# Kernel optimization log

Measured on AMD Instinct MI355X. Metric: run time of the kernel, lower is better.

The kernel has to match this reference:

```python
import jax, jax.numpy as jnp
import numpy as np

DIM = 96; NH = 3; WS = 7; SHIFT = 3; P = 5; H = 56; W = 56
HEAD = DIM // NH; SCALE = HEAD ** -0.5
NWH = H // WS; NWW = W // WS; NW = NWH * NWW
TP = P * NW                 # total prompts = 320
N = P + WS * WS             # tokens per window incl. prompts = 54
HIDDEN = int(DIM * 4.0)


def _rel_pos_index():
    coords = np.stack(np.meshgrid(np.arange(WS), np.arange(WS), indexing='ij'))
    cf = coords.reshape(2, -1)
    rel = (cf[:, :, None] - cf[:, None, :]).transpose(1, 2, 0).astype(np.int64)
    rel[..., 0] += WS - 1
    rel[..., 1] += WS - 1
    rel[..., 0] *= 2 * WS - 1
    return rel.sum(-1)  # (49, 49)


def _attn_mask():
    img = np.zeros((H, W))
    cnt = 0
    sl = (slice(0, -WS), slice(-WS, -SHIFT), slice(-SHIFT, None))
    for hs in sl:
        for wsl in sl:
            img[hs, wsl] = cnt
            cnt += 1
    mw = img.reshape(NWH, WS, NWW, WS).transpose(0, 2, 1, 3).reshape(NW, WS * WS)
    am = mw[:, None, :] - mw[:, :, None]
    am = np.where(am != 0, -100.0, 0.0).astype(np.float32)
    # zero-pad for prompt rows/cols, matching the torch code's cat of zeros
    return np.pad(am, ((0, 0), (P, 0), (P, 0)))  # (NW, N, N)


RPI = _rel_pos_index()
MASK = jnp.asarray(_attn_mask())


def _ln(x, g, b):
    m = x.mean(-1, keepdims=True)
    v = ((x - m) ** 2).mean(-1, keepdims=True)
    return (x - m) / jnp.sqrt(v + 1e-5) * g + b


def setup_inputs() -> dict:
    key = jax.random.key(0)
    ks = jax.random.split(key, 10)
    B = 64
    s = DIM ** -0.5
    return {
        'x': jax.random.normal(ks[0], (B, H * W + TP, DIM), jnp.float32),
        'norm1_g': jnp.ones((DIM,), jnp.float32),
        'norm1_b': jnp.zeros((DIM,), jnp.float32),
        'qkv_w': jax.random.normal(ks[1], (DIM, 3 * DIM), jnp.float32) * s,
        'qkv_b': jnp.zeros((3 * DIM,), jnp.float32),
        'rpb_table': jax.random.normal(ks[2], ((2 * WS - 1) ** 2, NH), jnp.float32) * 0.02,
        'proj_w': jax.random.normal(ks[3], (DIM, DIM), jnp.float32) * s,
        'proj_b': jnp.zeros((DIM,), jnp.float32),
        'norm2_g': jnp.ones((DIM,), jnp.float32),
        'norm2_b': jnp.zeros((DIM,), jnp.float32),
        'fc1_w': jax.random.normal(ks[4], (DIM, HIDDEN), jnp.float32) * s,
        'fc1_b': jnp.zeros((HIDDEN,), jnp.float32),
        'fc2_w': jax.random.normal(ks[5], (HIDDEN, DIM), jnp.float32) * (HIDDEN ** -0.5),
        'fc2_b': jnp.zeros((DIM,), jnp.float32),
    }


def _block(x, norm1_g, norm1_b, qkv_w, qkv_b, rpb_table, proj_w, proj_b,
           norm2_g, norm2_b, fc1_w, fc1_b, fc2_w, fc2_b):
    B = x.shape[0]
    shortcut = x
    xn = _ln(x, norm1_g, norm1_b)

    prompt = xn[:, :TP, :]                       # (B, NW*P, C)
    feat = xn[:, TP:, :].reshape(B, H, W, DIM)
    feat = jnp.roll(feat, (-SHIFT, -SHIFT), (1, 2))

    # window partition -> (B*NW, WS*WS, C)
    xw = feat.reshape(B, NWH, WS, NWW, WS, DIM).transpose(0, 1, 3, 2, 4, 5)
    xw = xw.reshape(B * NW, WS * WS, DIM)
    # prepend per-window prompts
    xw = jnp.concatenate([prompt.reshape(B * NW, P, DIM), xw], axis=1)  # (B*NW, N, C)

    # attention
    qkv = (xw @ qkv_w + qkv_b).reshape(B * NW, N, 3, NH, HEAD).transpose(2, 0, 3, 1, 4)
    q, k, v = qkv[0] * SCALE, qkv[1], qkv[2]     # (B*NW, NH, N, HEAD)
    attn = jnp.einsum('bhnd,bhmd->bhnm', q, k)

    bias = rpb_table[RPI.reshape(-1)].reshape(WS * WS, WS * WS, NH).transpose(2, 0, 1)
    bias = jnp.pad(bias, ((0, 0), (P, 0), (P, 0)))  # (NH, N, N)
    attn = attn + bias[None]

    attn = attn.reshape(B, NW, NH, N, N) + MASK[None, :, None]
    attn = jax.nn.softmax(attn.reshape(B * NW, NH, N, N), axis=-1)

    out = jnp.einsum('bhnm,bhmd->bhnd', attn, v).transpose(0, 2, 1, 3).reshape(B * NW, N, DIM)
    out = out @ proj_w + proj_b

    prompt_out = out[:, :P, :].reshape(B, TP, DIM)
    fo = out[:, P:, :].reshape(B, NWH, NWW, WS, WS, DIM).transpose(0, 1, 3, 2, 4, 5)
    fo = fo.reshape(B, H, W, DIM)
    fo = jnp.roll(fo, (SHIFT, SHIFT), (1, 2))

    y = jnp.concatenate([prompt_out, fo.reshape(B, H * W, DIM)], axis=1)
    y = shortcut + y

    h = _ln(y, norm2_g, norm2_b)
    h = jax.nn.gelu(h @ fc1_w + fc1_b, approximate=False)
    y = y + (h @ fc2_w + fc2_b)
    return y


def reference(x, norm1_g, norm1_b, qkv_w, qkv_b, rpb_table, proj_w, proj_b,
              norm2_g, norm2_b, fc1_w, fc1_b, fc2_w, fc2_b):
    return _block(x, norm1_g, norm1_b, qkv_w, qkv_b, rpb_table, proj_w, proj_b,
                  norm2_g, norm2_b, fc1_w, fc1_b, fc2_w, fc2_b)
```

## Files before the change

kernel.cpp:

```cpp
#include <hip/hip_runtime.h>
#include <cmath>

typedef __bf16 bf16x8 __attribute__((ext_vector_type(8)));
typedef __bf16 bf16x4 __attribute__((ext_vector_type(4)));
typedef float  f32x4  __attribute__((ext_vector_type(4)));

#define MFMA16(a,b,c) __builtin_amdgcn_mfma_f32_16x16x32_bf16((a),(b),(c),0,0,0)

#define SCALE_Q 0.17677669529663687f


#define KST 104
#define VP  68


__global__ __launch_bounds__(256) void prep(const float* __restrict__ qkv_w,
                                            const float* __restrict__ proj_w,
                                            const float* __restrict__ fc1_w,
                                            const float* __restrict__ fc2_w,
                                            const float* __restrict__ rpb,
                                            __bf16* __restrict__ ws,
                                            float* __restrict__ tbl)
{
    int i = blockIdx.x * 256 + threadIdx.x;
    {
        int j = i;
        if (j < 27648) {
            int c = j / 96, k = j % 96;
            float v = qkv_w[k * 288 + c];
            if (c < 96) v *= SCALE_Q;
            ws[j] = (__bf16)v;
        } else if ((j -= 27648) < 9216) {
            int c = j / 96, k = j % 96;
            ws[27648 + j] = (__bf16)proj_w[k * 96 + c];
        } else if ((j -= 9216) < 36864) {
            int c = j / 96, k = j % 96;
            ws[36864 + j] = (__bf16)fc1_w[k * 384 + c];
        } else if ((j -= 36864) < 36864) {
            int c = j / 384, k = j % 384;
            ws[73728 + j] = (__bf16)fc2_w[k * 96 + c];
        }
    }
    if (i < 49152) {
        int k_ = i & 63, q_ = (i >> 6) & 63, h = (i >> 12) % 3, cls = i / 12288;
        float v;
        if (k_ >= 54) {
            v = -1e30f;
        } else {
            v = 0.f;
            if (q_ >= 5 && q_ < 54 && k_ >= 5) {
                int an = q_ - 5, am = k_ - 5;
                int iy = an / 7, ix = an % 7, jy = am / 7, jx = am % 7;
                v = rpb[((iy - jy + 6) * 13 + (ix - jx + 6)) * 3 + h];
                int whp = cls >> 1, wwp = cls & 1;
                int idn = (whp ? (iy < 4 ? 1 : 2) : 0) * 3 + (wwp ? (ix < 4 ? 1 : 2) : 0);
                int idm = (whp ? (jy < 4 ? 1 : 2) : 0) * 3 + (wwp ? (jx < 4 ? 1 : 2) : 0);
                if (idn != idm) v -= 100.f;
            }
        }
        tbl[i] = v;
    }
}

__device__ __forceinline__ int src_index(int b, int w, int wh, int ww, int t)
{
    if (t < 5) return b * 3456 + w * 5 + t;
    int a = t - 5;
    int hi = wh * 7 + a / 7 + 3; if (hi >= 56) hi -= 56;
    int wi = ww * 7 + a % 7 + 3; if (wi >= 56) wi -= 56;
    return b * 3456 + 320 + hi * 56 + wi;
}

__global__ __launch_bounds__(256, 2) void block_fused(const float* __restrict__ x,
                                                  const float* __restrict__ n1g, const float* __restrict__ n1b,
                                                  const float* __restrict__ qkvb, const float* __restrict__ tbl,
                                                  const float* __restrict__ projb,
                                                  const float* __restrict__ n2g, const float* __restrict__ n2b,
                                                  const float* __restrict__ fc1b, const float* __restrict__ fc2b,
                                                  const __bf16* __restrict__ wqkvT, const __bf16* __restrict__ wprojT,
                                                  const __bf16* __restrict__ w1T, const __bf16* __restrict__ w2T,
                                                  float* __restrict__ out)
{
    __shared__ __align__(16) char smem[79360];

    const int tid  = threadIdx.x;
    const int lane = tid & 63;
    const int wv   = tid >> 6;
    const int l15  = lane & 15;
    const int quad = lane >> 4;

    const int g  = blockIdx.x;
    const int b  = g >> 5;
    const int wp = g & 31;

    const int trow = wv * 16 + l15;

    __bf16* kt[2];  __bf16* vTp[2];  __bf16* sw[2];
    int wI[2], whI[2], wwI[2], clsI[2], tsrc[2];
    #pragma unroll
    for (int wx = 0; wx < 2; wx++) {
        kt[wx]  = (__bf16*)(smem + wx * 13312);
        vTp[wx] = (__bf16*)(smem + 26624 + wx * 13056);
        sw[wx]  = (__bf16*)(smem + 52736 + (wv * 2 + wx) * 3328);
        int w = wp * 2 + wx;
        wI[wx] = w;  whI[wx] = w >> 3;  wwI[wx] = w & 7;
        clsI[wx] = ((whI[wx] == 7) ? 2 : 0) + ((wwI[wx] == 7) ? 1 : 0);
        tsrc[wx] = src_index(b, w, whI[wx], wwI[wx], trow < 54 ? trow : 53);
    }

    bf16x8 xnfr[2][3];
    {
        float xv[2][24];
        #pragma unroll
        for (int wx = 0; wx < 2; wx++) {
            if (trow < 54) {
                const float* xr = x + (size_t)tsrc[wx] * 96 + quad * 8;
                #pragma unroll
                for (int ks = 0; ks < 3; ks++) {
                    float4 a0 = *(const float4*)(xr + ks * 32);
                    float4 a1 = *(const float4*)(xr + ks * 32 + 4);
                    float* p = xv[wx] + ks * 8;
                    p[0]=a0.x; p[1]=a0.y; p[2]=a0.z; p[3]=a0.w;
                    p[4]=a1.x; p[5]=a1.y; p[6]=a1.z; p[7]=a1.w;
                }
            } else {
                #pragma unroll
                for (int j = 0; j < 24; j++) xv[wx][j] = 0.f;
            }
        }
        float s[2] = {0.f, 0.f}, sq[2] = {0.f, 0.f};
        #pragma unroll
        for (int wx = 0; wx < 2; wx++)
            #pragma unroll
            for (int j = 0; j < 24; j++) { s[wx] += xv[wx][j]; sq[wx] += xv[wx][j] * xv[wx][j]; }
        #pragma unroll
        for (int wx = 0; wx < 2; wx++) { s[wx] += __shfl_xor(s[wx], 16, 64); sq[wx] += __shfl_xor(sq[wx], 16, 64); }
        #pragma unroll
        for (int wx = 0; wx < 2; wx++) { s[wx] += __shfl_xor(s[wx], 32, 64); sq[wx] += __shfl_xor(sq[wx], 32, 64); }
        float keep = (trow < 54) ? 1.f : 0.f;
        #pragma unroll
        for (int wx = 0; wx < 2; wx++) {
            float mean = s[wx] * (1.f / 96.f);
            float rstd = rsqrtf(sq[wx] * (1.f / 96.f) - mean * mean + 1e-5f);
            #pragma unroll
            for (int ks = 0; ks < 3; ks++) {
                const float* gp = n1g + ks * 32 + quad * 8;
                const float* bp = n1b + ks * 32 + quad * 8;
                float4 g0 = *(const float4*)(gp), g1 = *(const float4*)(gp + 4);
                float4 b0 = *(const float4*)(bp), b1 = *(const float4*)(bp + 4);
                float gg[8] = {g0.x,g0.y,g0.z,g0.w,g1.x,g1.y,g1.z,g1.w};
                float bb[8] = {b0.x,b0.y,b0.z,b0.w,b1.x,b1.y,b1.z,b1.w};
                #pragma unroll
                for (int j = 0; j < 8; j++)
                    xnfr[wx][ks][j] = (__bf16)(((xv[wx][ks*8+j] - mean) * rstd * gg[j] + bb[j]) * keep);
            }
        }
    }

    #pragma unroll
    for (int nt = 0; nt < 12; nt++) {
        const __bf16* br = wqkvT + (size_t)(nt * 16 + l15) * 96 + quad * 8;
        bf16x8 b0 = *(const bf16x8*)(br);
        bf16x8 b1 = *(const bf16x8*)(br + 32);
        bf16x8 b2 = *(const bf16x8*)(br + 64);
        float4 bias4 = *(const float4*)(qkvb + nt * 16 + quad * 4);
        if (nt < 6) { bias4.x *= SCALE_Q; bias4.y *= SCALE_Q; bias4.z *= SCALE_Q; bias4.w *= SCALE_Q; }
        #pragma unroll
        for (int wx = 0; wx < 2; wx++) {
            f32x4 acc = {0.f, 0.f, 0.f, 0.f};
            acc = MFMA16(b0, xnfr[wx][0], acc);
            acc = MFMA16(b1, xnfr[wx][1], acc);
            acc = MFMA16(b2, xnfr[wx][2], acc);
            bf16x4 pk;
            pk[0] = (__bf16)(acc[0] + bias4.x);
            pk[1] = (__bf16)(acc[1] + bias4.y);
            pk[2] = (__bf16)(acc[2] + bias4.z);
            pk[3] = (__bf16)(acc[3] + bias4.w);
            if (nt < 6) *(bf16x4*)(sw[wx] + l15 * KST + nt * 16 + quad * 4) = pk;
            else        *(bf16x4*)(kt[wx] + (size_t)trow * KST + (nt - 6) * 16 + quad * 4) = pk;
        }
    }
    bf16x8 aq[2][3];
    #pragma unroll
    for (int wx = 0; wx < 2; wx++)
        #pragma unroll
        for (int h = 0; h < 3; h++)
            aq[wx][h] = *(const bf16x8*)(sw[wx] + l15 * KST + h * 32 + quad * 8);

    #pragma unroll
    for (int nt = 12; nt < 18; nt++) {
        const __bf16* br = wqkvT + (size_t)(nt * 16 + l15) * 96 + quad * 8;
        bf16x8 b0 = *(const bf16x8*)(br);
        bf16x8 b1 = *(const bf16x8*)(br + 32);
        bf16x8 b2 = *(const bf16x8*)(br + 64);
        float bias = qkvb[nt * 16 + l15];
        int vc = nt * 16 + l15 - 192;
        #pragma unroll
        for (int wx = 0; wx < 2; wx++) {
            f32x4 acc = {0.f, 0.f, 0.f, 0.f};
            acc = MFMA16(xnfr[wx][0], b0, acc);
            acc = MFMA16(xnfr[wx][1], b1, acc);
            acc = MFMA16(xnfr[wx][2], b2, acc);
            bf16x4 pk;
            pk[0] = (__bf16)(acc[0] + bias);
            pk[1] = (__bf16)(acc[1] + bias);
            pk[2] = (__bf16)(acc[2] + bias);
            pk[3] = (__bf16)(acc[3] + bias);
            *(bf16x4*)(vTp[wx] + (size_t)vc * VP + wv * 16 + quad * 4) = pk;
        }
    }
    __syncthreads();

    f32x4 oacc[2][6];
    #pragma unroll
    for (int wx = 0; wx < 2; wx++)
        #pragma unroll
        for (int i = 0; i < 6; i++) oacc[wx][i] = (f32x4){0.f, 0.f, 0.f, 0.f};

    #pragma unroll
    for (int h = 0; h < 3; h++) {
        float sv[2][4][4];
        #pragma unroll
        for (int wx = 0; wx < 2; wx++) {
            const float* tbh = tbl + (size_t)(clsI[wx] * 3 + h) * 4096 + trow * 64 + quad * 4;
            #pragma unroll
            for (int nt = 0; nt < 4; nt++) {
                bf16x8 ak = *(const bf16x8*)(kt[wx] + (nt * 16 + l15) * KST + h * 32 + quad * 8);
                f32x4 c = {0.f, 0.f, 0.f, 0.f};
                c = MFMA16(ak, aq[wx][h], c);
                float4 tv = *(const float4*)(tbh + nt * 16);
                sv[wx][nt][0] = c[0] + tv.x;
                sv[wx][nt][1] = c[1] + tv.y;
                sv[wx][nt][2] = c[2] + tv.z;
                sv[wx][nt][3] = c[3] + tv.w;
            }
        }
        #pragma unroll
        for (int wx = 0; wx < 2; wx++) {
            float mx = sv[wx][0][0];
            #pragma unroll
            for (int nt = 0; nt < 4; nt++)
                #pragma unroll
                for (int r = 0; r < 4; r++) mx = fmaxf(mx, sv[wx][nt][r]);
            mx = fmaxf(mx, __shfl_xor(mx, 16, 64));
            mx = fmaxf(mx, __shfl_xor(mx, 32, 64));
            float ps[4][4]; float sum = 0.f;
            #pragma unroll
            for (int nt = 0; nt < 4; nt++)
                #pragma unroll
                for (int r = 0; r < 4; r++) { ps[nt][r] = __expf(sv[wx][nt][r] - mx); sum += ps[nt][r]; }
            sum += __shfl_xor(sum, 16, 64);
            sum += __shfl_xor(sum, 32, 64);
            float inv = 1.f / sum;
            #pragma unroll
            for (int nt = 0; nt < 4; nt++) {
                bf16x4 pk;
                pk[0] = (__bf16)(ps[nt][0] * inv);
                pk[1] = (__bf16)(ps[nt][1] * inv);
                pk[2] = (__bf16)(ps[nt][2] * inv);
                pk[3] = (__bf16)(ps[nt][3] * inv);
                *(bf16x4*)(sw[wx] + l15 * KST + nt * 16 + quad * 4) = pk;
            }
        }
        #pragma unroll
        for (int wx = 0; wx < 2; wx++) {
            bf16x8 pa0 = *(const bf16x8*)(sw[wx] + l15 * KST + quad * 8);
            bf16x8 pa1 = *(const bf16x8*)(sw[wx] + l15 * KST + 32 + quad * 8);
            #pragma unroll
            for (int dt = 0; dt < 2; dt++) {
                const __bf16* vr = vTp[wx] + (h * 32 + dt * 16 + l15) * VP;
                f32x4 acc = oacc[wx][h * 2 + dt];
                acc = MFMA16(*(const bf16x8*)(vr + quad * 8), pa0, acc);
                acc = MFMA16(*(const bf16x8*)(vr + 32 + quad * 8), pa1, acc);
                oacc[wx][h * 2 + dt] = acc;
            }
        }
    }

    bf16x8 ofr[2][3];
    #pragma unroll
    for (int wx = 0; wx < 2; wx++) {
        #pragma unroll
        for (int i = 0; i < 6; i++) {
            bf16x4 pk;
            pk[0] = (__bf16)oacc[wx][i][0];
            pk[1] = (__bf16)oacc[wx][i][1];
            pk[2] = (__bf16)oacc[wx][i][2];
            pk[3] = (__bf16)oacc[wx][i][3];
            *(bf16x4*)(sw[wx] + l15 * KST + i * 16 + quad * 4) = pk;
        }
        #pragma unroll
        for (int ks = 0; ks < 3; ks++)
            ofr[wx][ks] = *(const bf16x8*)(sw[wx] + l15 * KST + ks * 32 + quad * 8);
    }

    float av[2][24];
    #pragma unroll
    for (int nt = 0; nt < 6; nt++) {
        const __bf16* br = wprojT + (size_t)(nt * 16 + l15) * 96 + quad * 8;
        bf16x8 b0 = *(const bf16x8*)(br);
        bf16x8 b1 = *(const bf16x8*)(br + 32);
        bf16x8 b2 = *(const bf16x8*)(br + 64);
        float4 pb = *(const float4*)(projb + nt * 16 + quad * 4);
        #pragma unroll
        for (int wx = 0; wx < 2; wx++) {
            f32x4 acc = {0.f, 0.f, 0.f, 0.f};
            acc = MFMA16(b0, ofr[wx][0], acc);
            acc = MFMA16(b1, ofr[wx][1], acc);
            acc = MFMA16(b2, ofr[wx][2], acc);
            av[wx][nt*4+0] = acc[0] + pb.x;
            av[wx][nt*4+1] = acc[1] + pb.y;
            av[wx][nt*4+2] = acc[2] + pb.z;
            av[wx][nt*4+3] = acc[3] + pb.w;
        }
    }

    float yv[2][24];
    float s2[2] = {0.f, 0.f}, sq2[2] = {0.f, 0.f};
    #pragma unroll
    for (int wx = 0; wx < 2; wx++) {
        const float* xr = x + (size_t)tsrc[wx] * 96 + quad * 4;
        #pragma unroll
        for (int nt = 0; nt < 6; nt++) {
            float4 xa = *(const float4*)(xr + nt * 16);
            float* yp = yv[wx] + nt * 4;
            yp[0] = xa.x + av[wx][nt*4+0];
            yp[1] = xa.y + av[wx][nt*4+1];
            yp[2] = xa.z + av[wx][nt*4+2];
            yp[3] = xa.w + av[wx][nt*4+3];
            #pragma unroll
            for (int j = 0; j < 4; j++) { s2[wx] += yp[j]; sq2[wx] += yp[j] * yp[j]; }
        }
    }
    #pragma unroll
    for (int wx = 0; wx < 2; wx++) { s2[wx] += __shfl_xor(s2[wx], 16, 64); sq2[wx] += __shfl_xor(sq2[wx], 16, 64); }
    #pragma unroll
    for (int wx = 0; wx < 2; wx++) { s2[wx] += __shfl_xor(s2[wx], 32, 64); sq2[wx] += __shfl_xor(sq2[wx], 32, 64); }

    bf16x8 afr[2][3];
    #pragma unroll
    for (int wx = 0; wx < 2; wx++) {
        float mean = s2[wx] * (1.f / 96.f);
        float rstd = rsqrtf(sq2[wx] * (1.f / 96.f) - mean * mean + 1e-5f);
        #pragma unroll
        for (int nt = 0; nt < 6; nt++) {
            float4 gg = *(const float4*)(n2g + nt * 16 + quad * 4);
            float4 bb = *(const float4*)(n2b + nt * 16 + quad * 4);
            bf16x4 pk;
            pk[0] = (__bf16)((yv[wx][nt*4+0] - mean) * rstd * gg.x + bb.x);
            pk[1] = (__bf16)((yv[wx][nt*4+1] - mean) * rstd * gg.y + bb.y);
            pk[2] = (__bf16)((yv[wx][nt*4+2] - mean) * rstd * gg.z + bb.z);
            pk[3] = (__bf16)((yv[wx][nt*4+3] - mean) * rstd * gg.w + bb.w);
            *(bf16x4*)(sw[wx] + l15 * KST + nt * 16 + quad * 4) = pk;
        }
        #pragma unroll
        for (int ks = 0; ks < 3; ks++)
            afr[wx][ks] = *(const bf16x8*)(sw[wx] + l15 * KST + ks * 32 + quad * 8);
    }

    f32x4 acc2[2][6];
    #pragma unroll
    for (int wx = 0; wx < 2; wx++)
        #pragma unroll
        for (int nt = 0; nt < 6; nt++) acc2[wx][nt] = (f32x4){0.f, 0.f, 0.f, 0.f};

    #pragma unroll
    for (int np = 0; np < 12; np++) {
        int reg = (np % 3) * 32;
        #pragma unroll
        for (int u = 0; u < 2; u++) {
            int ntx = np * 2 + u;
            const __bf16* br = w1T + (size_t)(ntx * 16 + l15) * 96 + quad * 8;
            bf16x8 b0 = *(const bf16x8*)(br);
            bf16x8 b1 = *(const bf16x8*)(br + 32);
            bf16x8 b2 = *(const bf16x8*)(br + 64);
            float4 fb = *(const float4*)(fc1b + ntx * 16 + quad * 4);
            float fbv[4] = {fb.x, fb.y, fb.z, fb.w};
            #pragma unroll
            for (int wx = 0; wx < 2; wx++) {
                f32x4 acc = {0.f, 0.f, 0.f, 0.f};
                acc = MFMA16(b0, afr[wx][0], acc);
                acc = MFMA16(b1, afr[wx][1], acc);
                acc = MFMA16(b2, afr[wx][2], acc);
                bf16x4 pk;
                #pragma unroll
                for (int r = 0; r < 4; r++) {
                    float v  = acc[r] + fbv[r];
                    float u2 = -1.5957691216057308f * v * (1.f + 0.044715f * v * v);
                    float t  = __expf(u2);
                    pk[r] = (__bf16)(v * __builtin_amdgcn_rcpf(1.f + t));
                }
                *(bf16x4*)(sw[wx] + l15 * KST + reg + u * 16 + quad * 4) = pk;
            }
        }
        bf16x8 hc0 = *(const bf16x8*)(sw[0] + l15 * KST + reg + quad * 8);
        bf16x8 hc1 = *(const bf16x8*)(sw[1] + l15 * KST + reg + quad * 8);
        #pragma unroll
        for (int nt = 0; nt < 6; nt++) {
            bf16x8 wb = *(const bf16x8*)(w2T + (size_t)(nt * 16 + l15) * 384 + np * 32 + quad * 8);
            acc2[0][nt] = MFMA16(wb, hc0, acc2[0][nt]);
            acc2[1][nt] = MFMA16(wb, hc1, acc2[1][nt]);
        }
    }

    #pragma unroll
    for (int nt = 0; nt < 6; nt++) {
        float4 fb = *(const float4*)(fc2b + nt * 16 + quad * 4);
        #pragma unroll
        for (int wx = 0; wx < 2; wx++) {
            if (trow < 54) {
                float4 o;
                o.x = yv[wx][nt*4+0] + acc2[wx][nt][0] + fb.x;
                o.y = yv[wx][nt*4+1] + acc2[wx][nt][1] + fb.y;
                o.z = yv[wx][nt*4+2] + acc2[wx][nt][2] + fb.z;
                o.w = yv[wx][nt*4+3] + acc2[wx][nt][3] + fb.w;
                *(float4*)(out + (size_t)tsrc[wx] * 96 + nt * 16 + quad * 4) = o;
            }
        }
    }
}

extern "C" void kernel_launch(void* const* d_in, const int* in_sizes, int n_in,
                              void* d_out, int out_size, void* d_ws, size_t ws_size,
                              hipStream_t stream)
{
    const float* x      = (const float*)d_in[0];
    const float* n1g    = (const float*)d_in[1];
    const float* n1b    = (const float*)d_in[2];
    const float* qkv_w  = (const float*)d_in[3];
    const float* qkv_b  = (const float*)d_in[4];
    const float* rpb    = (const float*)d_in[5];
    const float* proj_w = (const float*)d_in[6];
    const float* proj_b = (const float*)d_in[7];
    const float* n2g    = (const float*)d_in[8];
    const float* n2b    = (const float*)d_in[9];
    const float* fc1_w  = (const float*)d_in[10];
    const float* fc1_b  = (const float*)d_in[11];
    const float* fc2_w  = (const float*)d_in[12];
    const float* fc2_b  = (const float*)d_in[13];

    __bf16* ws     = (__bf16*)d_ws;
    __bf16* wqkvT  = ws;
    __bf16* wprojT = ws + 27648;
    __bf16* w1T    = ws + 36864;
    __bf16* w2T    = ws + 73728;
    float*  tbl    = (float*)((char*)d_ws + 221184);

    float* out = (float*)d_out;

    hipLaunchKernelGGL(prep, dim3(432), dim3(256), 0, stream,
                       qkv_w, proj_w, fc1_w, fc2_w, rpb, ws, tbl);
    hipLaunchKernelGGL(block_fused, dim3(2048), dim3(256), 0, stream,
                       x, n1g, n1b, qkv_b, tbl, proj_b, n2g, n2b, fc1_b, fc2_b,
                       wqkvT, wprojT, w1T, w2T, out);
}
```

Before: 358.5 us.

## Replace per-wave LDS transpose scratch with cross-lane shuffles, raise occupancy to 3

New measurement: 376.8 us. 1.05x slower.

```diff
diff --git a/kernel.cpp b/kernel.cpp
--- a/kernel.cpp
+++ b/kernel.cpp
@@ -4,15 +4,34 @@
 typedef __bf16 bf16x8 __attribute__((ext_vector_type(8)));
 typedef __bf16 bf16x4 __attribute__((ext_vector_type(4)));
 typedef float  f32x4  __attribute__((ext_vector_type(4)));
+typedef unsigned int u32;
 
 #define MFMA16(a,b,c) __builtin_amdgcn_mfma_f32_16x16x32_bf16((a),(b),(c),0,0,0)
 
 #define SCALE_Q 0.17677669529663687f
-
 
 #define KST 104
 #define VP  68
 
+
+union PK2 { bf16x4 v; u32 d[2]; };
+union FR8 { bf16x8 v; u32 d[4]; };
+
+__device__ __forceinline__ bf16x8 xpose(u32 A0, u32 A1, u32 B0, u32 B1, int b5, int b4)
+{
+    u32 s0 = b5 ? A0 : B0, s1 = b5 ? A1 : B1;
+    u32 x0 = (u32)__shfl_xor((int)s0, 32, 64);
+    u32 x1 = (u32)__shfl_xor((int)s1, 32, 64);
+    u32 t00 = b5 ? x0 : A0, t01 = b5 ? x1 : A1;
+    u32 t10 = b5 ? B0 : x0, t11 = b5 ? B1 : x1;
+    u32 r0 = b4 ? t00 : t10, r1 = b4 ? t01 : t11;
+    u32 y0 = (u32)__shfl_xor((int)r0, 16, 64);
+    u32 y1 = (u32)__shfl_xor((int)r1, 16, 64);
+    FR8 o;
+    o.d[0] = b4 ? y0 : t00;  o.d[1] = b4 ? y1 : t01;
+    o.d[2] = b4 ? t10 : y0;  o.d[3] = b4 ? t11 : y1;
+    return o.v;
+}
 
 __global__ __launch_bounds__(256) void prep(const float* __restrict__ qkv_w,
                                             const float* __restrict__ proj_w,
@@ -71,7 +90,7 @@
     return b * 3456 + 320 + hi * 56 + wi;
 }
 
-__global__ __launch_bounds__(256, 2) void block_fused(const float* __restrict__ x,
+__global__ __launch_bounds__(256, 3) void block_fused(const float* __restrict__ x,
                                                   const float* __restrict__ n1g, const float* __restrict__ n1b,
                                                   const float* __restrict__ qkvb, const float* __restrict__ tbl,
                                                   const float* __restrict__ projb,
@@ -81,13 +100,15 @@
                                                   const __bf16* __restrict__ w1T, const __bf16* __restrict__ w2T,
                                                   float* __restrict__ out)
 {
-    __shared__ __align__(16) char smem[79360];
+    __shared__ __align__(16) char smem[52736];
 
     const int tid  = threadIdx.x;
     const int lane = tid & 63;
     const int wv   = tid >> 6;
     const int l15  = lane & 15;
     const int quad = lane >> 4;
+    const int b5   = quad >> 1;
+    const int b4   = quad & 1;
 
     const int g  = blockIdx.x;
     const int b  = g >> 5;
@@ -95,13 +116,12 @@
 
     const int trow = wv * 16 + l15;
 
-    __bf16* kt[2];  __bf16* vTp[2];  __bf16* sw[2];
+    __bf16* kt[2];  __bf16* vTp[2];
     int wI[2], whI[2], wwI[2], clsI[2], tsrc[2];
     #pragma unroll
     for (int wx = 0; wx < 2; wx++) {
         kt[wx]  = (__bf16*)(smem + wx * 13312);
         vTp[wx] = (__bf16*)(smem + 26624 + wx * 13056);
-        sw[wx]  = (__bf16*)(smem + 52736 + (wv * 2 + wx) * 3328);
         int w = wp * 2 + wx;
         wI[wx] = w;  whI[wx] = w >> 3;  wwI[wx] = w & 7;
         clsI[wx] = ((whI[wx] == 7) ? 2 : 0) + ((wwI[wx] == 7) ? 1 : 0);
@@ -157,6 +177,7 @@
         }
     }
 
+    PK2 qd[2][6];
     #pragma unroll
     for (int nt = 0; nt < 12; nt++) {
         const __bf16* br = wqkvT + (size_t)(nt * 16 + l15) * 96 + quad * 8;
@@ -171,13 +192,13 @@
             acc = MFMA16(b0, xnfr[wx][0], acc);
             acc = MFMA16(b1, xnfr[wx][1], acc);
             acc = MFMA16(b2, xnfr[wx][2], acc);
-            bf16x4 pk;
-            pk[0] = (__bf16)(acc[0] + bias4.x);
-            pk[1] = (__bf16)(acc[1] + bias4.y);
-            pk[2] = (__bf16)(acc[2] + bias4.z);
-            pk[3] = (__bf16)(acc[3] + bias4.w);
-            if (nt < 6) *(bf16x4*)(sw[wx] + l15 * KST + nt * 16 + quad * 4) = pk;
-            else        *(bf16x4*)(kt[wx] + (size_t)trow * KST + (nt - 6) * 16 + quad * 4) = pk;
+            PK2 pk;
+            pk.v[0] = (__bf16)(acc[0] + bias4.x);
+            pk.v[1] = (__bf16)(acc[1] + bias4.y);
+            pk.v[2] = (__bf16)(acc[2] + bias4.z);
+            pk.v[3] = (__bf16)(acc[3] + bias4.w);
+            if (nt < 6) qd[wx][nt] = pk;
+            else        *(bf16x4*)(kt[wx] + (size_t)trow * KST + (nt - 6) * 16 + quad * 4) = pk.v;
         }
     }
     bf16x8 aq[2][3];
@@ -185,7 +206,8 @@
     for (int wx = 0; wx < 2; wx++)
         #pragma unroll
         for (int h = 0; h < 3; h++)
-            aq[wx][h] = *(const bf16x8*)(sw[wx] + l15 * KST + h * 32 + quad * 8);
+            aq[wx][h] = xpose(qd[wx][2*h].d[0], qd[wx][2*h].d[1],
+                              qd[wx][2*h+1].d[0], qd[wx][2*h+1].d[1], b5, b4);
 
     #pragma unroll
     for (int nt = 12; nt < 18; nt++) {
@@ -235,6 +257,7 @@
                 sv[wx][nt][3] = c[3] + tv.w;
             }
         }
+        PK2 pp[2][4];
         #pragma unroll
         for (int wx = 0; wx < 2; wx++) {
             float mx = sv[wx][0][0];
@@ -254,18 +277,16 @@
             float inv = 1.f / sum;
             #pragma unroll
             for (int nt = 0; nt < 4; nt++) {
-                bf16x4 pk;
-                pk[0] = (__bf16)(ps[nt][0] * inv);
-                pk[1] = (__bf16)(ps[nt][1] * inv);
-                pk[2] = (__bf16)(ps[nt][2] * inv);
-                pk[3] = (__bf16)(ps[nt][3] * inv);
-                *(bf16x4*)(sw[wx] + l15 * KST + nt * 16 + quad * 4) = pk;
-            }
-        }
-        #pragma unroll
-        for (int wx = 0; wx < 2; wx++) {
-            bf16x8 pa0 = *(const bf16x8*)(sw[wx] + l15 * KST + quad * 8);
-            bf16x8 pa1 = *(const bf16x8*)(sw[wx] + l15 * KST + 32 + quad * 8);
+                pp[wx][nt].v[0] = (__bf16)(ps[nt][0] * inv);
+                pp[wx][nt].v[1] = (__bf16)(ps[nt][1] * inv);
+                pp[wx][nt].v[2] = (__bf16)(ps[nt][2] * inv);
+                pp[wx][nt].v[3] = (__bf16)(ps[nt][3] * inv);
+            }
+        }
+        #pragma unroll
+        for (int wx = 0; wx < 2; wx++) {
+            bf16x8 pa0 = xpose(pp[wx][0].d[0], pp[wx][0].d[1], pp[wx][1].d[0], pp[wx][1].d[1], b5, b4);
+            bf16x8 pa1 = xpose(pp[wx][2].d[0], pp[wx][2].d[1], pp[wx][3].d[0], pp[wx][3].d[1], b5, b4);
             #pragma unroll
             for (int dt = 0; dt < 2; dt++) {
                 const __bf16* vr = vTp[wx] + (h * 32 + dt * 16 + l15) * VP;
@@ -280,18 +301,17 @@
     bf16x8 ofr[2][3];
     #pragma unroll
     for (int wx = 0; wx < 2; wx++) {
+        PK2 po[6];
         #pragma unroll
         for (int i = 0; i < 6; i++) {
-            bf16x4 pk;
-            pk[0] = (__bf16)oacc[wx][i][0];
-            pk[1] = (__bf16)oacc[wx][i][1];
-            pk[2] = (__bf16)oacc[wx][i][2];
-            pk[3] = (__bf16)oacc[wx][i][3];
-            *(bf16x4*)(sw[wx] + l15 * KST + i * 16 + quad * 4) = pk;
+            po[i].v[0] = (__bf16)oacc[wx][i][0];
+            po[i].v[1] = (__bf16)oacc[wx][i][1];
+            po[i].v[2] = (__bf16)oacc[wx][i][2];
+            po[i].v[3] = (__bf16)oacc[wx][i][3];
         }
         #pragma unroll
         for (int ks = 0; ks < 3; ks++)
-            ofr[wx][ks] = *(const bf16x8*)(sw[wx] + l15 * KST + ks * 32 + quad * 8);
+            ofr[wx][ks] = xpose(po[2*ks].d[0], po[2*ks].d[1], po[2*ks+1].d[0], po[2*ks+1].d[1], b5, b4);
     }
 
     float av[2][24];
@@ -342,20 +362,19 @@
     for (int wx = 0; wx < 2; wx++) {
         float mean = s2[wx] * (1.f / 96.f);
         float rstd = rsqrtf(sq2[wx] * (1.f / 96.f) - mean * mean + 1e-5f);
+        PK2 py[6];
         #pragma unroll
         for (int nt = 0; nt < 6; nt++) {
             float4 gg = *(const float4*)(n2g + nt * 16 + quad * 4);
             float4 bb = *(const float4*)(n2b + nt * 16 + quad * 4);
-            bf16x4 pk;
-            pk[0] = (__bf16)((yv[wx][nt*4+0] - mean) * rstd * gg.x + bb.x);
-            pk[1] = (__bf16)((yv[wx][nt*4+1] - mean) * rstd * gg.y + bb.y);
-            pk[2] = (__bf16)((yv[wx][nt*4+2] - mean) * rstd * gg.z + bb.z);
-            pk[3] = (__bf16)((yv[wx][nt*4+3] - mean) * rstd * gg.w + bb.w);
-            *(bf16x4*)(sw[wx] + l15 * KST + nt * 16 + quad * 4) = pk;
+            py[nt].v[0] = (__bf16)((yv[wx][nt*4+0] - mean) * rstd * gg.x + bb.x);
+            py[nt].v[1] = (__bf16)((yv[wx][nt*4+1] - mean) * rstd * gg.y + bb.y);
+            py[nt].v[2] = (__bf16)((yv[wx][nt*4+2] - mean) * rstd * gg.z + bb.z);
+            py[nt].v[3] = (__bf16)((yv[wx][nt*4+3] - mean) * rstd * gg.w + bb.w);
         }
         #pragma unroll
         for (int ks = 0; ks < 3; ks++)
-            afr[wx][ks] = *(const bf16x8*)(sw[wx] + l15 * KST + ks * 32 + quad * 8);
+            afr[wx][ks] = xpose(py[2*ks].d[0], py[2*ks].d[1], py[2*ks+1].d[0], py[2*ks+1].d[1], b5, b4);
     }
 
     f32x4 acc2[2][6];
@@ -366,7 +385,7 @@
 
     #pragma unroll
     for (int np = 0; np < 12; np++) {
-        int reg = (np % 3) * 32;
+        PK2 pg[2][2];
         #pragma unroll
         for (int u = 0; u < 2; u++) {
             int ntx = np * 2 + u;
@@ -382,19 +401,17 @@
                 acc = MFMA16(b0, afr[wx][0], acc);
                 acc = MFMA16(b1, afr[wx][1], acc);
                 acc = MFMA16(b2, afr[wx][2], acc);
-                bf16x4 pk;
                 #pragma unroll
                 for (int r = 0; r < 4; r++) {
                     float v  = acc[r] + fbv[r];
                     float u2 = -1.5957691216057308f * v * (1.f + 0.044715f * v * v);
                     float t  = __expf(u2);
-                    pk[r] = (__bf16)(v * __builtin_amdgcn_rcpf(1.f + t));
+                    pg[wx][u].v[r] = (__bf16)(v * __builtin_amdgcn_rcpf(1.f + t));
                 }
-                *(bf16x4*)(sw[wx] + l15 * KST + reg + u * 16 + quad * 4) = pk;
-            }
-        }
-        bf16x8 hc0 = *(const bf16x8*)(sw[0] + l15 * KST + reg + quad * 8);
-        bf16x8 hc1 = *(const bf16x8*)(sw[1] + l15 * KST + reg + quad * 8);
+            }
+        }
+        bf16x8 hc0 = xpose(pg[0][0].d[0], pg[0][0].d[1], pg[0][1].d[0], pg[0][1].d[1], b5, b4);
+        bf16x8 hc1 = xpose(pg[1][0].d[0], pg[1][0].d[1], pg[1][1].d[0], pg[1][1].d[1], b5, b4);
         #pragma unroll
         for (int nt = 0; nt < 6; nt++) {
             bf16x8 wb = *(const bf16x8*)(w2T + (size_t)(nt * 16 + l15) * 384 + np * 32 + quad * 8);
```
